# Kernel tuning notes

Hardware: AMD Instinct MI355X
Metric: run time of the kernel (lower is better)

Reference implementation:

```python
import math
import jax, jax.numpy as jnp
import numpy as np

B, N_IN, C_IN = 32, 16384, 64
IMG = 128            # sqrt(N_IN)
E_BR = 64            # embed_dim per PRM branch
DILATIONS = (1, 2, 3)
DIM = E_BR * len(DILATIONS)   # 192, attn input dim
EMB = 64             # token_dims * head_cnt
M_FEAT = int(EMB * 0.5)       # 32 performer random features
EPS = 1e-8


def setup_inputs() -> dict:
    key = jax.random.key(0)
    ks = jax.random.split(key, 12)
    x = jax.random.normal(ks[0], (B, N_IN, C_IN), jnp.float32)
    # PRM: one conv per dilation, weights stacked [nb, O, I, kh, kw] (OIHW)
    conv_w = jax.random.normal(ks[1], (len(DILATIONS), E_BR, C_IN, 3, 3), jnp.float32) * 0.05
    conv_b = jax.random.normal(ks[2], (len(DILATIONS), E_BR), jnp.float32) * 0.01
    ln1_g = jnp.ones((DIM,), jnp.float32)
    ln1_b = jnp.zeros((DIM,), jnp.float32)
    kqv_w = jax.random.normal(ks[3], (DIM, 3 * EMB), jnp.float32) * 0.02
    kqv_b = jnp.zeros((3 * EMB,), jnp.float32)
    proj_w = jax.random.normal(ks[4], (EMB, EMB), jnp.float32) * 0.02
    proj_b = jnp.zeros((EMB,), jnp.float32)
    # performer random-feature matrix: orthogonal rows, scaled by sqrt(m) (non-trainable)
    rng = np.random.default_rng(0)
    q, _ = np.linalg.qr(rng.standard_normal((EMB, M_FEAT)))
    w_perf = jnp.asarray(q.T * math.sqrt(M_FEAT), jnp.float32)  # [m, emb]
    ln2_g = jnp.ones((EMB,), jnp.float32)
    ln2_b = jnp.zeros((EMB,), jnp.float32)
    mlp_w1 = jax.random.normal(ks[5], (EMB, EMB), jnp.float32) * 0.02
    mlp_b1 = jnp.zeros((EMB,), jnp.float32)
    mlp_w2 = jax.random.normal(ks[6], (EMB, EMB), jnp.float32) * 0.02
    mlp_b2 = jnp.zeros((EMB,), jnp.float32)
    return dict(x=x, conv_w=conv_w, conv_b=conv_b, ln1_g=ln1_g, ln1_b=ln1_b,
                kqv_w=kqv_w, kqv_b=kqv_b, proj_w=proj_w, proj_b=proj_b,
                w_perf=w_perf, ln2_g=ln2_g, ln2_b=ln2_b,
                mlp_w1=mlp_w1, mlp_b1=mlp_b1, mlp_w2=mlp_w2, mlp_b2=mlp_b2)


def _layernorm(x, g, b):
    mu = jnp.mean(x, axis=-1, keepdims=True)
    var = jnp.var(x, axis=-1, keepdims=True)
    return (x - mu) * jax.lax.rsqrt(var + 1e-5) * g + b


def _prm_exp(t, w):
    # t: [B, T, emb], w: [m, emb] -> exp(w.t - |t|^2/2) / sqrt(m)
    xd = 0.5 * jnp.sum(t * t, axis=-1, keepdims=True)       # [B, T, 1]
    wtx = jnp.einsum('btd,md->btm', t, w)                    # [B, T, m]
    return jnp.exp(wtx - xd) / math.sqrt(w.shape[0])


def reference(x, conv_w, conv_b, ln1_g, ln1_b, kqv_w, kqv_b, proj_w, proj_b,
              w_perf, ln2_g, ln2_b, mlp_w1, mlp_b1, mlp_w2, mlp_b2):
    Bx, N, C = x.shape
    # x.permute(0,2,1) then reshape to image NCHW
    img = jnp.transpose(x, (0, 2, 1)).reshape(Bx, C, IMG, IMG)
    # PRM: multi-dilation strided convs + GELU, channel-concat (branch-major)
    ys = []
    for i, d in enumerate(DILATIONS):
        pad = d  # ceil(((k-1)*d + 1 - stride)/2) for k=3, stride=2
        y = jax.lax.conv_general_dilated(
            img, conv_w[i], window_strides=(2, 2),
            padding=[(pad, pad), (pad, pad)], rhs_dilation=(d, d),
            dimension_numbers=('NCHW', 'OIHW', 'NCHW'))
        y = y + conv_b[i][None, :, None, None]
        ys.append(jax.nn.gelu(y, approximate=False))
    y = jnp.concatenate(ys, axis=1)                          # [B, 3*E, H', W']
    tokens = jnp.transpose(y.reshape(Bx, DIM, -1), (0, 2, 1))  # [B, T, 192]

    # Token_performer.attn on norm1(tokens)
    h = _layernorm(tokens, ln1_g, ln1_b)
    kqv = h @ kqv_w + kqv_b                                  # [B, T, 3*emb]
    k, q, v = jnp.split(kqv, 3, axis=-1)                     # split order: k, q, v
    kp = _prm_exp(k, w_perf)                                 # [B, T, m]
    qp = _prm_exp(q, w_perf)                                 # [B, T, m]
    D = jnp.einsum('btm,bm->bt', qp, jnp.sum(kp, axis=1))[..., None]   # [B, T, 1]
    kptv = jnp.einsum('btd,btm->bdm', v, kp)                 # [B, emb, m]
    yatt = jnp.einsum('btm,bdm->btd', qp, kptv) / (D + EPS)  # [B, T, emb]
    yatt = v + (yatt @ proj_w + proj_b)                      # skip inside single_attn (dropout=id at eval)

    # x = x + drop_path(mlp(norm2(x))) ; drop_path/dropout = identity at eval
    h2 = _layernorm(yatt, ln2_g, ln2_b)
    h2 = jax.nn.gelu(h2 @ mlp_w1 + mlp_b1, approximate=False) @ mlp_w2 + mlp_b2
    return yatt + h2
```

## Files before the change

kernel.cpp:

```cpp
#include <hip/hip_runtime.h>
#include <hip/hip_bf16.h>


#define TOK 4096
#define NB  32

typedef __attribute__((ext_vector_type(8)))  short short8;
typedef __attribute__((ext_vector_type(4)))  short short4v;
typedef __attribute__((ext_vector_type(16))) float f32x16;

__device__ __forceinline__ float gelu_fast(float v) {
    float u = v * fmaf(0.0713548162f, v * v, 1.5957691216f);
    float e = __expf(-u);
    return v * __builtin_amdgcn_rcpf(1.f + e);
}

__device__ __forceinline__ short f2bf(float f) {
    __hip_bfloat16 h = __float2bfloat16(f);
    return *reinterpret_cast<short*>(&h);
}

__device__ __forceinline__ float bf2f(short s) {
    union { unsigned u; float f; } x;
    x.u = ((unsigned)(unsigned short)s) << 16;
    return x.f;
}

__global__ __launch_bounds__(256) void k_prep(
        const float* __restrict__ cw, const float* __restrict__ kw,
        const float* __restrict__ pw, const float* __restrict__ w1,
        const float* __restrict__ w2m, const float* __restrict__ wperf,
        short* __restrict__ w2c, short* __restrict__ kwbf,
        short* __restrict__ pTbf, short* __restrict__ w1bf,
        short* __restrict__ w2bf, short* __restrict__ wpbf) {
    int idx = blockIdx.x * 256 + threadIdx.x;
    if (idx < 110592) {
        int c = idx & 63;
        int t = idx >> 6;
        int e = t & 63;
        int tap = t >> 6;
        int kwi = tap % 3, t2 = tap / 3;
        int r = t2 % 3, brr = t2 / 3;
        float v = cw[(((brr * 64 + e) * 64 + c) * 3 + r) * 3 + kwi];
        int dst = ((((brr * 9 + r * 3 + kwi) * 4 + (c >> 4)) * 2 + ((c >> 3) & 1)) * 64 + e) * 8 + (c & 7);
        w2c[dst] = f2bf(v);
    } else if (idx < 147456) {
        int i2 = idx - 110592;
        int o = i2 / 192, i = i2 % 192;
        int dst = (((i >> 4) * 2 + ((i >> 3) & 1)) * 192 + o) * 8 + (i & 7);
        kwbf[dst] = f2bf(kw[i * 192 + o]);
    } else if (idx < 151552) {
        int i2 = idx - 147456;
        int o = i2 >> 6, d = i2 & 63;
        int dst = (((d >> 4) * 2 + ((d >> 3) & 1)) * 64 + o) * 8 + (d & 7);
        pTbf[dst] = f2bf(pw[d * 64 + o]);
    } else if (idx < 155648) {
        int i2 = idx - 151552;
        int i = i2 >> 6, jd = i2 & 63;
        int dst = (((jd >> 4) * 2 + ((jd >> 3) & 1)) * 64 + i) * 8 + (jd & 7);
        w1bf[dst] = f2bf(w1[jd * 64 + i]);
    } else if (idx < 159744) {
        int i2 = idx - 155648;
        int o = i2 >> 6, i = i2 & 63;
        int dst = (((i >> 4) * 2 + ((i >> 3) & 1)) * 64 + o) * 8 + (i & 7);
        w2bf[dst] = f2bf(w2m[i * 64 + o]);
    } else if (idx < 161792) {
        int i2 = idx - 159744;
        int m = i2 >> 6, d = i2 & 63;
        int dst = (((d >> 4) * 2 + ((d >> 3) & 1)) * 32 + m) * 8 + (d & 7);
        wpbf[dst] = f2bf(wperf[m * 64 + d]);
    }
}

__global__ __launch_bounds__(256) void k_conv6(
        const float* __restrict__ x, const short* __restrict__ w2c,
        const float* __restrict__ cb, short* __restrict__ tokens) {
    const int wg  = blockIdx.x;
    const int swz_id = (wg & 7) * 768 + (wg >> 3);
    const int b   = swz_id / 192;
    const int rem = swz_id - b * 192;
    const int oh  = rem / 3;
    const int br  = rem - oh * 3;
    const int d   = br + 1;
    const int tid = threadIdx.x;
    const int lane = tid & 63;
    const int wv = tid >> 6;
    const int cl = lane & 31;
    const int g  = lane >> 5;
    const int wm = wv & 1;
    const int wn = wv >> 1;

    __shared__ short sA[3 * 68 * 2 * 32];

    const int ow = wm * 32 + cl;
    const int ecol = wn * 32 + cl;
    const short* wbr = w2c + br * 9 * 4096;

    f32x16 acc = {0.f, 0.f, 0.f, 0.f, 0.f, 0.f, 0.f, 0.f,
                  0.f, 0.f, 0.f, 0.f, 0.f, 0.f, 0.f, 0.f};

    for (int h = 0; h < 2; ++h) {
        if (h == 0 && tid < 96) {
            int s16 = tid & 7;
            int ii  = (tid >> 3) & 3;
            int r   = tid >> 5;
            int i   = (ii < 2) ? ii : (64 + ii);
            short8 z = {0, 0, 0, 0, 0, 0, 0, 0};
            *(short8*)((char*)sA + (r * 68 + i) * 128 + s16 * 16) = z;
        }
        for (int it = 0; it < 6; ++it) {
            int flat = it * 256 + tid;
            int c8l = flat & 3;
            int iw  = (flat >> 2) & 127;
            int r   = flat >> 9;
            int ih  = 2 * oh + (r - 1) * d;
            int iw4 = iw + 4;
            int i   = iw4 >> 1;
            int p   = iw4 & 1;
            char* dst = (char*)sA + (r * 68 + i) * 128
                      + ((((p * 4 + c8l) * 16)) ^ ((i & 7) << 4));
            if ((unsigned)ih < 128u) {
                const float* src = x + ((size_t)(b * 16384 + ih * 128 + iw)) * 64
                                 + h * 32 + c8l * 8;
                float4 f0 = *(const float4*)(src);
                float4 f1 = *(const float4*)(src + 4);
                short8 v;
                v[0] = f2bf(f0.x); v[1] = f2bf(f0.y); v[2] = f2bf(f0.z); v[3] = f2bf(f0.w);
                v[4] = f2bf(f1.x); v[5] = f2bf(f1.y); v[6] = f2bf(f1.z); v[7] = f2bf(f1.w);
                *(short8*)dst = v;
            } else {
                short8 z = {0, 0, 0, 0, 0, 0, 0, 0};
                *(short8*)dst = z;
            }
        }
        __syncthreads();

#pragma unroll
        for (int r = 0; r < 3; ++r) {
#pragma unroll
            for (int kwi = 0; kwi < 3; ++kwi) {
                const int iw4 = 2 * ow + (kwi - 1) * d + 4;
                const int i   = iw4 >> 1;
                const int p   = iw4 & 1;
                const char* arow = (const char*)sA + (r * 68 + i) * 128;
                const int swzk = (i & 7) << 4;
                const short* wt = wbr + (r * 3 + kwi) * 4096;
#pragma unroll
                for (int kk = 0; kk < 2; ++kk) {
                    const int ks = h * 2 + kk;
                    short8 a = *(const short8*)(arow + ((((p * 4 + kk * 2 + g) * 16)) ^ swzk));
                    short8 bf = *(const short8*)(wt + ((ks * 2 + g) * 64 + ecol) * 8);
                    acc = __builtin_amdgcn_mfma_f32_32x32x16_bf16(a, bf, acc, 0, 0, 0);
                }
            }
        }
        __syncthreads();
    }

    const int eG = br * 64 + wn * 32 + cl;
    const float bias = cb[eG];
    short* outb = tokens + ((size_t)(b * TOK + oh * 64 + wm * 32)) * 192 + eG;
#pragma unroll
    for (int reg = 0; reg < 16; ++reg) {
        int owl = (reg & 3) + 8 * (reg >> 2) + 4 * g;
        outb[(size_t)owl * 192] = f2bf(gelu_fast(acc[reg] + bias));
    }
}

__global__ __launch_bounds__(256) void k_lnkqvp(
        const short* __restrict__ tokens, const float* __restrict__ g,
        const float* __restrict__ be, const short* __restrict__ wbf,
        const float* __restrict__ bias, const short* __restrict__ wpbf,
        short* __restrict__ vT, short* __restrict__ kpT,
        short* __restrict__ qpT) {
    const int b = blockIdx.y;
    const int t0 = blockIdx.x * 64;
    const int tid = threadIdx.x;

    __shared__ short sB[64 * 192];
    __shared__ float red[64 * 8];
    __shared__ float xdk[128];
    __shared__ float xdq[128];

    const int r = tid >> 2, q = tid & 3;
    const short* rowp = tokens + ((size_t)(b * TOK + t0 + r)) * 192 + q * 48;
    float v[48];
    float s1 = 0.f, s2 = 0.f;
#pragma unroll
    for (int i = 0; i < 6; ++i) {
        short8 x8 = *(const short8*)(rowp + i * 8);
#pragma unroll
        for (int j = 0; j < 8; ++j) {
            float f = bf2f(x8[j]);
            v[i * 8 + j] = f;
            s1 += f;
            s2 = fmaf(f, f, s2);
        }
    }
    red[r * 8 + q] = s1;
    red[r * 8 + 4 + q] = s2;
    __syncthreads();
    const float m1 = red[r * 8 + 0] + red[r * 8 + 1] + red[r * 8 + 2] + red[r * 8 + 3];
    const float m2 = red[r * 8 + 4] + red[r * 8 + 5] + red[r * 8 + 6] + red[r * 8 + 7];
    const float mu = m1 * (1.f / 192.f);
    const float var = m2 * (1.f / 192.f) - mu * mu;
    const float rs = rsqrtf(fmaxf(var, 0.f) + 1e-5f);
    const float4* g4 = (const float4*)(g + q * 48);
    const float4* b4 = (const float4*)(be + q * 48);
    char* rowB = (char*)sB + r * 384;
    const int swz = (r & 7) << 4;
#pragma unroll
    for (int i = 0; i < 12; ++i) {
        float4 gg = g4[i], bb = b4[i];
        short4v pk;
        pk.x = f2bf((v[4 * i + 0] - mu) * rs * gg.x + bb.x);
        pk.y = f2bf((v[4 * i + 1] - mu) * rs * gg.y + bb.y);
        pk.z = f2bf((v[4 * i + 2] - mu) * rs * gg.z + bb.z);
        pk.w = f2bf((v[4 * i + 3] - mu) * rs * gg.w + bb.w);
        *(short4v*)(rowB + (((q * 48 + i * 4) * 2) ^ swz)) = pk;
    }
    __syncthreads();

    const int lane = tid & 63;
    const int wv = tid >> 6;
    const int tt = wv & 1;
    const int wo = wv >> 1;
    const int colL = lane & 31;
    const int gq = lane >> 5;

    f32x16 acc0 = {0.f, 0.f, 0.f, 0.f, 0.f, 0.f, 0.f, 0.f,
                   0.f, 0.f, 0.f, 0.f, 0.f, 0.f, 0.f, 0.f};
    f32x16 acc1 = acc0, acc2 = acc0;
    const char* bbase = (const char*)sB + (tt * 32 + colL) * 384;
    const int bswz = ((tt * 32 + colL) & 7) << 4;
    const int ocol = wo * 32 + colL;

    for (int kk = 0; kk < 12; ++kk) {
        short8 bf = *(const short8*)(bbase + (((kk * 16 + gq * 8) * 2) ^ bswz));
        const short* ak = wbf + ((kk * 2 + gq) * 192 + ocol) * 8;
        short8 a0 = *(const short8*)(ak);
        short8 a1 = *(const short8*)(ak + 64 * 8);
        short8 a2 = *(const short8*)(ak + 128 * 8);
        acc0 = __builtin_amdgcn_mfma_f32_32x32x16_bf16(a0, bf, acc0, 0, 0, 0);
        acc1 = __builtin_amdgcn_mfma_f32_32x32x16_bf16(a1, bf, acc1, 0, 0, 0);
        acc2 = __builtin_amdgcn_mfma_f32_32x32x16_bf16(a2, bf, acc2, 0, 0, 0);
    }

    const int tl = tt * 32 + colL;
    const int tglob = t0 + tl;

    float kb[16], qb[16];
    float sk = 0.f, sq = 0.f;
    {
        short* vb = vT + (size_t)b * 64 * TOK + tglob;
#pragma unroll
        for (int reg = 0; reg < 16; ++reg) {
            int orow = (reg & 3) + 8 * (reg >> 2) + 4 * gq;
            int d = wo * 32 + orow;
            kb[reg] = acc0[reg] + bias[d];
            qb[reg] = acc1[reg] + bias[64 + d];
            float vv = acc2[reg] + bias[128 + d];
            vb[(size_t)d * TOK] = f2bf(vv);
            sk = fmaf(kb[reg], kb[reg], sk);
            sq = fmaf(qb[reg], qb[reg], sq);
        }
    }
    sk += __shfl_xor(sk, 32, 64);
    sq += __shfl_xor(sq, 32, 64);
    __syncthreads();

    if (gq == 0) {
        xdk[wo * 64 + tl] = 0.5f * sk;
        xdq[wo * 64 + tl] = 0.5f * sq;
    }
    {
        char* kS = (char*)sB;
        char* qS = (char*)sB + 8192;
        const int tswz = (tl & 7) << 4;
#pragma unroll
        for (int rq = 0; rq < 4; ++rq) {
            int d0 = wo * 32 + 8 * rq + 4 * gq;
            short4v pk, pq;
#pragma unroll
            for (int j = 0; j < 4; ++j) {
                ((short*)&pk)[j] = f2bf(kb[rq * 4 + j]);
                ((short*)&pq)[j] = f2bf(qb[rq * 4 + j]);
            }
            *(short4v*)(kS + tl * 128 + ((d0 * 2) ^ tswz)) = pk;
            *(short4v*)(qS + tl * 128 + ((d0 * 2) ^ tswz)) = pq;
        }
    }
    __syncthreads();

    {
        const int pass = wv >> 1;
        const int tt2 = wv & 1;
        const char* S = (char*)sB + pass * 8192;
        const int t2 = tt2 * 32 + colL;
        const int t2swz = (t2 & 7) << 4;
        f32x16 pacc = {0.f, 0.f, 0.f, 0.f, 0.f, 0.f, 0.f, 0.f,
                       0.f, 0.f, 0.f, 0.f, 0.f, 0.f, 0.f, 0.f};
#pragma unroll
        for (int ks = 0; ks < 4; ++ks) {
            short8 a = *(const short8*)(wpbf + ((ks * 2 + gq) * 32 + colL) * 8);
            short8 bb = *(const short8*)(S + t2 * 128 + (((ks * 16 + gq * 8) * 2) ^ t2swz));
            pacc = __builtin_amdgcn_mfma_f32_32x32x16_bf16(a, bb, pacc, 0, 0, 0);
        }
        const float* xda = pass ? xdq : xdk;
        const float xdv = xda[t2] + xda[64 + t2];
        short* dst = (pass ? qpT : kpT) + (size_t)b * 32 * TOK + t0 + t2;
#pragma unroll
        for (int reg = 0; reg < 16; ++reg) {
            int m = (reg & 3) + 8 * (reg >> 2) + 4 * gq;
            float kpv = __expf(pacc[reg] - xdv) * 0.17677669529663687f;
            dst[(size_t)m * TOK] = f2bf(kpv);
        }
    }
}

__global__ __launch_bounds__(256) void k_kptv(
        const short* __restrict__ vT, const short* __restrict__ kpT,
        float* __restrict__ kvp, float* __restrict__ skpp) {
    const int b = blockIdx.y, ch = blockIdx.x, tid = threadIdx.x;
    const int t = ch * 256 + tid;
    __shared__ float sv[256 * 65 + 256 * 36];
    float* skp = sv + 256 * 65;
    for (int dd = 0; dd < 64; ++dd)
        sv[tid * 65 + dd] = bf2f(vT[((size_t)(b * 64 + dd)) * TOK + t]);
    for (int m = 0; m < 32; ++m)
        skp[tid * 36 + m] = bf2f(kpT[((size_t)(b * 32 + m)) * TOK + t]);
    __syncthreads();

    const int dd = tid & 63;
    const int mg = __builtin_amdgcn_readfirstlane(tid >> 6);
    float acc[8];
#pragma unroll
    for (int j = 0; j < 8; ++j) acc[j] = 0.f;
    for (int tt = 0; tt < 256; ++tt) {
        float vv = sv[tt * 65 + dd];
        const float4* kq = (const float4*)(skp + tt * 36 + mg * 8);
        float4 a0 = kq[0], a1 = kq[1];
        acc[0] = fmaf(vv, a0.x, acc[0]);
        acc[1] = fmaf(vv, a0.y, acc[1]);
        acc[2] = fmaf(vv, a0.z, acc[2]);
        acc[3] = fmaf(vv, a0.w, acc[3]);
        acc[4] = fmaf(vv, a1.x, acc[4]);
        acc[5] = fmaf(vv, a1.y, acc[5]);
        acc[6] = fmaf(vv, a1.z, acc[6]);
        acc[7] = fmaf(vv, a1.w, acc[7]);
    }
    float* dst = kvp + (((size_t)(b * 16 + ch) * 64 + dd) * 32) + mg * 8;
#pragma unroll
    for (int j = 0; j < 8; ++j) dst[j] = acc[j];

    if (tid < 32) {
        float s = 0.f;
        for (int tt = 0; tt < 256; ++tt) s += skp[tt * 36 + tid];
        skpp[(b * 16 + ch) * 32 + tid] = s;
    }
}

__global__ __launch_bounds__(256) void k_reduce2(
        const float* __restrict__ kvp, const float* __restrict__ skpp,
        short* __restrict__ kvbf, float* __restrict__ sum_kp) {
    int idx = blockIdx.x * 256 + threadIdx.x;
    if (idx < 65536) {
        int b = idx >> 11, rem = idx & 2047, dd = rem >> 5, m = rem & 31;
        float s = 0.f;
        for (int ch = 0; ch < 16; ++ch) s += kvp[((b * 16 + ch) * 64 + dd) * 32 + m];
        int dst = (((b * 2 + (m >> 4)) * 2 + ((m >> 3) & 1)) * 64 + dd) * 8 + (m & 7);
        kvbf[dst] = f2bf(s);
    } else if (idx < 65536 + 1024) {
        int i = idx - 65536;
        int b = i >> 5, m = i & 31;
        float s = 0.f;
        for (int ch = 0; ch < 16; ++ch) s += skpp[(b * 16 + ch) * 32 + m];
        sum_kp[i] = s;
    }
}

__global__ __launch_bounds__(256) void k_fuse(
        const short* __restrict__ vT, const short* __restrict__ qpT,
        const short* __restrict__ kvbf, const float* __restrict__ sum_kp,
        const short* __restrict__ pTbf, const float* __restrict__ proj_b,
        const float* __restrict__ g2, const float* __restrict__ b2ln,
        const short* __restrict__ w1bf, const float* __restrict__ b1,
        const short* __restrict__ w2bf, const float* __restrict__ b2,
        float* __restrict__ out) {
    const int b = blockIdx.y;
    const int t0 = blockIdx.x * 64;
    const int tid = threadIdx.x;
    const int lane = tid & 63;
    const int cl = lane & 31;
    const int g  = lane >> 5;
    const int wv = tid >> 6;
    const int wr = wv & 1;
    const int wc = wv >> 1;

    __shared__ __align__(16) char pool[29952];
    short* qpS  = (short*)(pool + 0);
    short* ytS  = (short*)(pool + 5120);
    short* xnS  = (short*)(pool + 14336);
    short* hgS  = (short*)(pool + 0);
    float* outS = (float*)(pool + 9216);
    float* red  = (float*)(pool + 26624);
    float* stat = (float*)(pool + 27648);
    float* coefS= (float*)(pool + 28672);

    if (tid < 64) {
        coefS[tid]       = proj_b[tid];
        coefS[64 + tid]  = g2[tid];
        coefS[128 + tid] = b2ln[tid];
        coefS[192 + tid] = b1[tid];
        coefS[256 + tid] = b2[tid];
    }
    {
        const int t = tid & 63, q = tid >> 6;
        const float* sk = sum_kp + b * 32;
        float dsum = 0.f;
        short8 pk;
#pragma unroll
        for (int i = 0; i < 8; ++i) {
            int m = q * 8 + i;
            short s = qpT[((size_t)(b * 32 + m)) * TOK + t0 + t];
            dsum = fmaf(bf2f(s), sk[m], dsum);
            pk[i] = s;
        }
        *(short8*)(qpS + t * 40 + q * 8) = pk;
        red[t * 4 + q] = dsum;
    }
    __syncthreads();

    const int tl = wc * 32 + cl;
    const int tg = t0 + tl;
    const int rcol = wr * 32 + cl;

    f32x16 acc = {0.f, 0.f, 0.f, 0.f, 0.f, 0.f, 0.f, 0.f,
                  0.f, 0.f, 0.f, 0.f, 0.f, 0.f, 0.f, 0.f};
    {
        const short* Ab = kvbf + (size_t)b * 2048;
        short8 a0 = *(const short8*)(Ab + (g * 64 + rcol) * 8);
        short8 a1 = *(const short8*)(Ab + ((2 + g) * 64 + rcol) * 8);
        short8 b0 = *(const short8*)(qpS + tl * 40 + g * 8);
        short8 b1v = *(const short8*)(qpS + tl * 40 + 16 + g * 8);
        acc = __builtin_amdgcn_mfma_f32_32x32x16_bf16(a0, b0, acc, 0, 0, 0);
        acc = __builtin_amdgcn_mfma_f32_32x32x16_bf16(a1, b1v, acc, 0, 0, 0);
    }
    {
        float Dv = red[tl * 4 + 0] + red[tl * 4 + 1] + red[tl * 4 + 2] + red[tl * 4 + 3];
        float rD = 1.f / (Dv + 1e-8f);
#pragma unroll
        for (int rq = 0; rq < 4; ++rq) {
            int d0 = wr * 32 + 8 * rq + 4 * g;
            short4v p;
            p.x = f2bf(acc[rq * 4 + 0] * rD);
            p.y = f2bf(acc[rq * 4 + 1] * rD);
            p.z = f2bf(acc[rq * 4 + 2] * rD);
            p.w = f2bf(acc[rq * 4 + 3] * rD);
            *(short4v*)(ytS + tl * 72 + d0) = p;
        }
    }
    __syncthreads();

    f32x16 acc2 = {0.f, 0.f, 0.f, 0.f, 0.f, 0.f, 0.f, 0.f,
                   0.f, 0.f, 0.f, 0.f, 0.f, 0.f, 0.f, 0.f};
    {
#pragma unroll
        for (int ks = 0; ks < 4; ++ks) {
            short8 a = *(const short8*)(pTbf + ((ks * 2 + g) * 64 + rcol) * 8);
            short8 bb = *(const short8*)(ytS + tl * 72 + ks * 16 + g * 8);
            acc2 = __builtin_amdgcn_mfma_f32_32x32x16_bf16(a, bb, acc2, 0, 0, 0);
        }
    }
    float skv[16];
    {
        const short* vb = vT + (size_t)b * 64 * TOK + tg;
#pragma unroll
        for (int reg = 0; reg < 16; ++reg) {
            int o = wr * 32 + (reg & 3) + 8 * (reg >> 2) + 4 * g;
            skv[reg] = acc2[reg] + bf2f(vb[(size_t)o * TOK]) + coefS[o];
        }
    }

    {
        float s1 = 0.f, s2 = 0.f;
#pragma unroll
        for (int reg = 0; reg < 16; ++reg) {
            s1 += skv[reg];
            s2 = fmaf(skv[reg], skv[reg], s2);
        }
        s1 += __shfl_xor(s1, 32, 64);
        s2 += __shfl_xor(s2, 32, 64);
        if (g == 0) {
            stat[(wr * 64 + tl) * 2 + 0] = s1;
            stat[(wr * 64 + tl) * 2 + 1] = s2;
        }
        __syncthreads();
        float S1 = s1 + stat[((wr ^ 1) * 64 + tl) * 2 + 0];
        float S2 = s2 + stat[((wr ^ 1) * 64 + tl) * 2 + 1];
        float mu = S1 * (1.f / 64.f);
        float var = S2 * (1.f / 64.f) - mu * mu;
        float rs = rsqrtf(fmaxf(var, 0.f) + 1e-5f);
#pragma unroll
        for (int rq = 0; rq < 4; ++rq) {
            int o0 = wr * 32 + 8 * rq + 4 * g;
            short4v p;
#pragma unroll
            for (int j = 0; j < 4; ++j) {
                int o = o0 + j;
                float xn = (skv[rq * 4 + j] - mu) * rs * coefS[64 + o] + coefS[128 + o];
                ((short*)&p)[j] = f2bf(xn);
            }
            *(short4v*)(xnS + tl * 72 + o0) = p;
        }
    }
    __syncthreads();

    f32x16 acc3 = {0.f, 0.f, 0.f, 0.f, 0.f, 0.f, 0.f, 0.f,
                   0.f, 0.f, 0.f, 0.f, 0.f, 0.f, 0.f, 0.f};
    {
#pragma unroll
        for (int ks = 0; ks < 4; ++ks) {
            short8 a = *(const short8*)(w1bf + ((ks * 2 + g) * 64 + rcol) * 8);
            short8 bb = *(const short8*)(xnS + tl * 72 + ks * 16 + g * 8);
            acc3 = __builtin_amdgcn_mfma_f32_32x32x16_bf16(a, bb, acc3, 0, 0, 0);
        }
    }
    __syncthreads();
    {
#pragma unroll
        for (int rq = 0; rq < 4; ++rq) {
            int i0 = wr * 32 + 8 * rq + 4 * g;
            short4v p;
#pragma unroll
            for (int j = 0; j < 4; ++j) {
                int i = i0 + j;
                float hgv = gelu_fast(acc3[rq * 4 + j] + coefS[192 + i]);
                ((short*)&p)[j] = f2bf(hgv);
            }
            *(short4v*)(hgS + tl * 72 + i0) = p;
        }
    }
    __syncthreads();

    f32x16 acc4 = {0.f, 0.f, 0.f, 0.f, 0.f, 0.f, 0.f, 0.f,
                   0.f, 0.f, 0.f, 0.f, 0.f, 0.f, 0.f, 0.f};
    {
#pragma unroll
        for (int ks = 0; ks < 4; ++ks) {
            short8 a = *(const short8*)(w2bf + ((ks * 2 + g) * 64 + rcol) * 8);
            short8 bb = *(const short8*)(hgS + tl * 72 + ks * 16 + g * 8);
            acc4 = __builtin_amdgcn_mfma_f32_32x32x16_bf16(a, bb, acc4, 0, 0, 0);
        }
    }
    {
#pragma unroll
        for (int rq = 0; rq < 4; ++rq) {
            int o0 = wr * 32 + 8 * rq + 4 * g;
            float4 f;
#pragma unroll
            for (int j = 0; j < 4; ++j) {
                int o = o0 + j;
                ((float*)&f)[j] = skv[rq * 4 + j] + acc4[rq * 4 + j] + coefS[256 + o];
            }
            *(float4*)(outS + tl * 68 + o0) = f;
        }
    }
    __syncthreads();

    {
        const int tt = tid >> 2, qq = tid & 3;
        float* ob = out + ((size_t)(b * TOK) + t0 + tt) * 64;
#pragma unroll
        for (int it = 0; it < 4; ++it) {
            *(float4*)(ob + it * 16 + qq * 4) =
                *(float4*)(outS + tt * 68 + it * 16 + qq * 4);
        }
    }
}

extern "C" void kernel_launch(void* const* d_in, const int* in_sizes, int n_in,
                              void* d_out, int out_size, void* d_ws, size_t ws_size,
                              hipStream_t stream) {
    const float* x      = (const float*)d_in[0];
    const float* conv_w = (const float*)d_in[1];
    const float* conv_b = (const float*)d_in[2];
    const float* ln1_g  = (const float*)d_in[3];
    const float* ln1_b  = (const float*)d_in[4];
    const float* kqv_w  = (const float*)d_in[5];
    const float* kqv_b  = (const float*)d_in[6];
    const float* proj_w = (const float*)d_in[7];
    const float* proj_b = (const float*)d_in[8];
    const float* w_perf = (const float*)d_in[9];
    const float* ln2_g  = (const float*)d_in[10];
    const float* ln2_b  = (const float*)d_in[11];
    const float* mlp_w1 = (const float*)d_in[12];
    const float* mlp_b1 = (const float*)d_in[13];
    const float* mlp_w2 = (const float*)d_in[14];
    const float* mlp_b2 = (const float*)d_in[15];

    float* ws = (float*)d_ws;
    short* w2c    = (short*)ws;
    short* kwbf   = (short*)(ws + 55296);
    short* pTbf   = (short*)(ws + 73728);
    short* w1bf   = (short*)(ws + 75776);
    short* w2bf   = (short*)(ws + 77824);
    short* wpbf   = (short*)(ws + 79872);
    float* sum_kp = ws + 80896;
    short* kvbf   = (short*)(ws + 81920);
    short* tokens = (short*)(ws + 114688);
    float* wsB    = ws + 114688 + 12582912;
    short* vT     = (short*)wsB;
    short* qpT    = (short*)(wsB + 4194304);
    short* kpT    = (short*)(wsB + 6291456);
    float* skpp   = wsB + 8388608;
    float* kvp    = wsB + 8404992;
    float* outp   = (float*)d_out;

    k_prep   <<<632, 256, 0, stream>>>(conv_w, kqv_w, proj_w, mlp_w1, mlp_w2,
                                       w_perf, w2c, kwbf, pTbf, w1bf, w2bf, wpbf);
    k_conv6  <<<6144, 256, 0, stream>>>(x, w2c, conv_b, tokens);
    k_lnkqvp <<<dim3(64, 32), 256, 0, stream>>>(tokens, ln1_g, ln1_b, kwbf,
                                                kqv_b, wpbf, vT, kpT, qpT);
    k_kptv   <<<dim3(16, 32), 256, 0, stream>>>(vT, kpT, kvp, skpp);
    k_reduce2<<<260, 256, 0, stream>>>(kvp, skpp, kvbf, sum_kp);
    k_fuse   <<<dim3(64, 32), 256, 0, stream>>>(vT, qpT, kvbf, sum_kp,
                                                pTbf, proj_b, ln2_g, ln2_b,
                                                w1bf, mlp_b1, w2bf, mlp_b2, outp);
}
```

Before: 154.6 us.

## Compute two output rows per conv workgroup to reuse weight fragments

The dilated-conv kernel now has each workgroup produce two adjacent output rows with two accumulators, halving the grid. Each weight fragment loaded from global memory is reused for two MFMAs, and the channel loop is split into four phases of 16 channels with a new LDS layout and swizzle. This cuts redundant weight loads and per-workgroup overhead. In exchange there are more barriers per workgroup, more registers, and fewer workgroups to hide latency.

```diff
diff --git a/kernel.cpp b/kernel.cpp
--- a/kernel.cpp
+++ b/kernel.cpp
@@ -72,15 +72,16 @@
     }
 }
 
-__global__ __launch_bounds__(256) void k_conv6(
+__global__ __launch_bounds__(256) void k_conv7(
         const float* __restrict__ x, const short* __restrict__ w2c,
         const float* __restrict__ cb, short* __restrict__ tokens) {
     const int wg  = blockIdx.x;
-    const int swz_id = (wg & 7) * 768 + (wg >> 3);
-    const int b   = swz_id / 192;
-    const int rem = swz_id - b * 192;
-    const int oh  = rem / 3;
-    const int br  = rem - oh * 3;
+    const int swz_id = (wg & 7) * 384 + (wg >> 3);
+    const int b   = swz_id / 96;
+    const int rem = swz_id - b * 96;
+    const int ohp = rem / 3;
+    const int br  = rem - ohp * 3;
+    const int oh0 = ohp * 2;
     const int d   = br + 1;
     const int tid = threadIdx.x;
     const int lane = tid & 63;
@@ -90,38 +91,41 @@
     const int wm = wv & 1;
     const int wn = wv >> 1;
 
-    __shared__ short sA[3 * 68 * 2 * 32];
+    __shared__ short sA[6 * 34 * 64];
 
     const int ow = wm * 32 + cl;
     const int ecol = wn * 32 + cl;
     const short* wbr = w2c + br * 9 * 4096;
 
-    f32x16 acc = {0.f, 0.f, 0.f, 0.f, 0.f, 0.f, 0.f, 0.f,
-                  0.f, 0.f, 0.f, 0.f, 0.f, 0.f, 0.f, 0.f};
-
-    for (int h = 0; h < 2; ++h) {
-        if (h == 0 && tid < 96) {
-            int s16 = tid & 7;
-            int ii  = (tid >> 3) & 3;
-            int r   = tid >> 5;
-            int i   = (ii < 2) ? ii : (64 + ii);
-            short8 z = {0, 0, 0, 0, 0, 0, 0, 0};
-            *(short8*)((char*)sA + (r * 68 + i) * 128 + s16 * 16) = z;
-        }
+    f32x16 acc0 = {0.f, 0.f, 0.f, 0.f, 0.f, 0.f, 0.f, 0.f,
+                   0.f, 0.f, 0.f, 0.f, 0.f, 0.f, 0.f, 0.f};
+    f32x16 acc1 = acc0;
+
+    if (tid < 96) {
+        int slot = tid & 7;
+        int lsel = (tid >> 3) & 1;
+        int s    = tid >> 4;
+        int l    = lsel ? 33 : 0;
+        short8 z = {0, 0, 0, 0, 0, 0, 0, 0};
+        *(short8*)((char*)sA + (s * 34 + l) * 128 + slot * 16) = z;
+    }
+
+    for (int ph = 0; ph < 4; ++ph) {
         for (int it = 0; it < 6; ++it) {
             int flat = it * 256 + tid;
-            int c8l = flat & 3;
-            int iw  = (flat >> 2) & 127;
-            int r   = flat >> 9;
-            int ih  = 2 * oh + (r - 1) * d;
+            int c8 = flat & 1;
+            int iw = (flat >> 1) & 127;
+            int s  = flat >> 8;
+            int ohl = (s >= 3) ? 1 : 0;
+            int r   = s - ohl * 3;
+            int ih  = 2 * (oh0 + ohl) + (r - 1) * d;
             int iw4 = iw + 4;
-            int i   = iw4 >> 1;
-            int p   = iw4 & 1;
-            char* dst = (char*)sA + (r * 68 + i) * 128
-                      + ((((p * 4 + c8l) * 16)) ^ ((i & 7) << 4));
+            int l   = iw4 >> 2;
+            int slot = ((iw4 & 3) * 2 + c8) ^ (l & 7);
+            char* dst = (char*)sA + (s * 34 + l) * 128 + slot * 16;
             if ((unsigned)ih < 128u) {
                 const float* src = x + ((size_t)(b * 16384 + ih * 128 + iw)) * 64
-                                 + h * 32 + c8l * 8;
+                                 + ph * 16 + c8 * 8;
                 float4 f0 = *(const float4*)(src);
                 float4 f1 = *(const float4*)(src + 4);
                 short8 v;
@@ -139,18 +143,19 @@
         for (int r = 0; r < 3; ++r) {
 #pragma unroll
             for (int kwi = 0; kwi < 3; ++kwi) {
+                const short* wt = wbr + (r * 3 + kwi) * 4096;
+                short8 bfr = *(const short8*)(wt + ((ph * 2 + g) * 64 + ecol) * 8);
                 const int iw4 = 2 * ow + (kwi - 1) * d + 4;
-                const int i   = iw4 >> 1;
-                const int p   = iw4 & 1;
-                const char* arow = (const char*)sA + (r * 68 + i) * 128;
-                const int swzk = (i & 7) << 4;
-                const short* wt = wbr + (r * 3 + kwi) * 4096;
-#pragma unroll
-                for (int kk = 0; kk < 2; ++kk) {
-                    const int ks = h * 2 + kk;
-                    short8 a = *(const short8*)(arow + ((((p * 4 + kk * 2 + g) * 16)) ^ swzk));
-                    short8 bf = *(const short8*)(wt + ((ks * 2 + g) * 64 + ecol) * 8);
-                    acc = __builtin_amdgcn_mfma_f32_32x32x16_bf16(a, bf, acc, 0, 0, 0);
+                const int l   = iw4 >> 2;
+                const int slot = ((iw4 & 3) * 2 + g) ^ (l & 7);
+#pragma unroll
+                for (int ohl = 0; ohl < 2; ++ohl) {
+                    const int s = ohl * 3 + r;
+                    short8 a = *(const short8*)((char*)sA + (s * 34 + l) * 128 + slot * 16);
+                    if (ohl == 0)
+                        acc0 = __builtin_amdgcn_mfma_f32_32x32x16_bf16(a, bfr, acc0, 0, 0, 0);
+                    else
+                        acc1 = __builtin_amdgcn_mfma_f32_32x32x16_bf16(a, bfr, acc1, 0, 0, 0);
                 }
             }
         }
@@ -159,11 +164,21 @@
 
     const int eG = br * 64 + wn * 32 + cl;
     const float bias = cb[eG];
-    short* outb = tokens + ((size_t)(b * TOK + oh * 64 + wm * 32)) * 192 + eG;
-#pragma unroll
-    for (int reg = 0; reg < 16; ++reg) {
-        int owl = (reg & 3) + 8 * (reg >> 2) + 4 * g;
-        outb[(size_t)owl * 192] = f2bf(gelu_fast(acc[reg] + bias));
+    {
+        short* outb = tokens + ((size_t)(b * TOK + oh0 * 64 + wm * 32)) * 192 + eG;
+#pragma unroll
+        for (int reg = 0; reg < 16; ++reg) {
+            int owl = (reg & 3) + 8 * (reg >> 2) + 4 * g;
+            outb[(size_t)owl * 192] = f2bf(gelu_fast(acc0[reg] + bias));
+        }
+    }
+    {
+        short* outb = tokens + ((size_t)(b * TOK + (oh0 + 1) * 64 + wm * 32)) * 192 + eG;
+#pragma unroll
+        for (int reg = 0; reg < 16; ++reg) {
+            int owl = (reg & 3) + 8 * (reg >> 2) + 4 * g;
+            outb[(size_t)owl * 192] = f2bf(gelu_fast(acc1[reg] + bias));
+        }
     }
 }
 
@@ -619,7 +634,7 @@
 
     k_prep   <<<632, 256, 0, stream>>>(conv_w, kqv_w, proj_w, mlp_w1, mlp_w2,
                                        w_perf, w2c, kwbf, pTbf, w1bf, w2bf, wpbf);
-    k_conv6  <<<6144, 256, 0, stream>>>(x, w2c, conv_b, tokens);
+    k_conv7  <<<3072, 256, 0, stream>>>(x, w2c, conv_b, tokens);
     k_lnkqvp <<<dim3(64, 32), 256, 0, stream>>>(tokens, ln1_g, ln1_b, kwbf,
                                                 kqv_b, wpbf, vT, kpT, qpT);
     k_kptv   <<<dim3(16, 32), 256, 0, stream>>>(vT, kpT, kvp, skpp);
```

New measurement: 170.4 us. 10.2% more time.

## Pre-convert input to bf16 parity-split layout and drop LDS staging in conv

Applied to the files above, without the earlier changes.

Adds a pass that converts the fp32 input once into a bf16 layout split by column parity and channel slab. The conv kernel then loads MFMA A fragments directly from global memory, with no shared-memory staging or barriers, and zeros out-of-range taps with predication. This targets repeated fp32 reads and conversions across workgroups that share input rows. In exchange it adds a full extra write/read of the bf16 copy and uses strided global loads that depend on cache hits.

```diff
diff --git a/kernel.cpp b/kernel.cpp
--- a/kernel.cpp
+++ b/kernel.cpp
@@ -72,8 +72,34 @@
     }
 }
 
-__global__ __launch_bounds__(256) void k_conv6(
-        const float* __restrict__ x, const short* __restrict__ w2c,
+__global__ __launch_bounds__(256) void k_cvt2(
+        const float* __restrict__ x, short* __restrict__ xT) {
+    const int ih = blockIdx.x;
+    const int b  = blockIdx.y;
+    const float* rb = x + ((size_t)(b * 16384 + ih * 128)) * 64;
+    short* ob = xT + (size_t)(b * 128 + ih) * 8192;
+    const int tid = threadIdx.x;
+#pragma unroll
+    for (int it = 0; it < 4; ++it) {
+        int f = it * 256 + tid;
+        int j   = f & 7;
+        int s   = (f >> 3) & 7;
+        int whi = (f >> 6) & 7;
+        int par = f >> 9;
+        int iw2 = whi * 8 + j;
+        int iw  = 2 * iw2 + par;
+        const float* src = rb + iw * 64 + s * 8;
+        float4 f0 = *(const float4*)(src);
+        float4 f1 = *(const float4*)(src + 4);
+        short8 v;
+        v[0] = f2bf(f0.x); v[1] = f2bf(f0.y); v[2] = f2bf(f0.z); v[3] = f2bf(f0.w);
+        v[4] = f2bf(f1.x); v[5] = f2bf(f1.y); v[6] = f2bf(f1.z); v[7] = f2bf(f1.w);
+        *(short8*)(ob + ((par * 8 + s) * 64 + iw2) * 8) = v;
+    }
+}
+
+__global__ __launch_bounds__(256) void k_conv8(
+        const short* __restrict__ xT, const short* __restrict__ w2c,
         const float* __restrict__ cb, short* __restrict__ tokens) {
     const int wg  = blockIdx.x;
     const int swz_id = (wg & 7) * 768 + (wg >> 3);
@@ -89,72 +115,37 @@
     const int g  = lane >> 5;
     const int wm = wv & 1;
     const int wn = wv >> 1;
-
-    __shared__ short sA[3 * 68 * 2 * 32];
-
     const int ow = wm * 32 + cl;
     const int ecol = wn * 32 + cl;
     const short* wbr = w2c + br * 9 * 4096;
+    const short8 z8 = {0, 0, 0, 0, 0, 0, 0, 0};
 
     f32x16 acc = {0.f, 0.f, 0.f, 0.f, 0.f, 0.f, 0.f, 0.f,
                   0.f, 0.f, 0.f, 0.f, 0.f, 0.f, 0.f, 0.f};
 
-    for (int h = 0; h < 2; ++h) {
-        if (h == 0 && tid < 96) {
-            int s16 = tid & 7;
-            int ii  = (tid >> 3) & 3;
-            int r   = tid >> 5;
-            int i   = (ii < 2) ? ii : (64 + ii);
-            short8 z = {0, 0, 0, 0, 0, 0, 0, 0};
-            *(short8*)((char*)sA + (r * 68 + i) * 128 + s16 * 16) = z;
-        }
-        for (int it = 0; it < 6; ++it) {
-            int flat = it * 256 + tid;
-            int c8l = flat & 3;
-            int iw  = (flat >> 2) & 127;
-            int r   = flat >> 9;
-            int ih  = 2 * oh + (r - 1) * d;
-            int iw4 = iw + 4;
-            int i   = iw4 >> 1;
-            int p   = iw4 & 1;
-            char* dst = (char*)sA + (r * 68 + i) * 128
-                      + ((((p * 4 + c8l) * 16)) ^ ((i & 7) << 4));
-            if ((unsigned)ih < 128u) {
-                const float* src = x + ((size_t)(b * 16384 + ih * 128 + iw)) * 64
-                                 + h * 32 + c8l * 8;
-                float4 f0 = *(const float4*)(src);
-                float4 f1 = *(const float4*)(src + 4);
-                short8 v;
-                v[0] = f2bf(f0.x); v[1] = f2bf(f0.y); v[2] = f2bf(f0.z); v[3] = f2bf(f0.w);
-                v[4] = f2bf(f1.x); v[5] = f2bf(f1.y); v[6] = f2bf(f1.z); v[7] = f2bf(f1.w);
-                *(short8*)dst = v;
-            } else {
-                short8 z = {0, 0, 0, 0, 0, 0, 0, 0};
-                *(short8*)dst = z;
+#pragma unroll
+    for (int r = 0; r < 3; ++r) {
+        const int ih = 2 * oh + (r - 1) * d;
+        const bool rv = (unsigned)ih < 128u;
+        const int ihc = ih & 127;
+        const short* rowb = xT + (size_t)(b * 128 + ihc) * 8192;
+#pragma unroll
+        for (int kwi = 0; kwi < 3; ++kwi) {
+            const int o = (kwi - 1) * d;
+            const int par = o & 1;
+            const int iw2 = ow + ((o - par) >> 1);
+            const bool va = rv && ((unsigned)iw2 < 64u);
+            const int iw2c = iw2 & 63;
+            const short* abase = rowb + par * 4096 + iw2c * 8;
+            const short* wt = wbr + (r * 3 + kwi) * 4096;
+#pragma unroll
+            for (int ks = 0; ks < 4; ++ks) {
+                short8 a = *(const short8*)(abase + (ks * 2 + g) * 512);
+                if (!va) a = z8;
+                short8 bf = *(const short8*)(wt + ((ks * 2 + g) * 64 + ecol) * 8);
+                acc = __builtin_amdgcn_mfma_f32_32x32x16_bf16(a, bf, acc, 0, 0, 0);
             }
         }
-        __syncthreads();
-
-#pragma unroll
-        for (int r = 0; r < 3; ++r) {
-#pragma unroll
-            for (int kwi = 0; kwi < 3; ++kwi) {
-                const int iw4 = 2 * ow + (kwi - 1) * d + 4;
-                const int i   = iw4 >> 1;
-                const int p   = iw4 & 1;
-                const char* arow = (const char*)sA + (r * 68 + i) * 128;
-                const int swzk = (i & 7) << 4;
-                const short* wt = wbr + (r * 3 + kwi) * 4096;
-#pragma unroll
-                for (int kk = 0; kk < 2; ++kk) {
-                    const int ks = h * 2 + kk;
-                    short8 a = *(const short8*)(arow + ((((p * 4 + kk * 2 + g) * 16)) ^ swzk));
-                    short8 bf = *(const short8*)(wt + ((ks * 2 + g) * 64 + ecol) * 8);
-                    acc = __builtin_amdgcn_mfma_f32_32x32x16_bf16(a, bf, acc, 0, 0, 0);
-                }
-            }
-        }
-        __syncthreads();
     }
 
     const int eG = br * 64 + wn * 32 + cl;
@@ -615,11 +606,13 @@
     short* kpT    = (short*)(wsB + 6291456);
     float* skpp   = wsB + 8388608;
     float* kvp    = wsB + 8404992;
+    short* xT     = (short*)(ws + 114688 + 12582912 + 9453568);
     float* outp   = (float*)d_out;
 
     k_prep   <<<632, 256, 0, stream>>>(conv_w, kqv_w, proj_w, mlp_w1, mlp_w2,
                                        w_perf, w2c, kwbf, pTbf, w1bf, w2bf, wpbf);
-    k_conv6  <<<6144, 256, 0, stream>>>(x, w2c, conv_b, tokens);
+    k_cvt2   <<<dim3(128, 32), 256, 0, stream>>>(x, xT);
+    k_conv8  <<<6144, 256, 0, stream>>>(xT, w2c, conv_b, tokens);
     k_lnkqvp <<<dim3(64, 32), 256, 0, stream>>>(tokens, ln1_g, ln1_b, kwbf,
                                                 kqv_b, wpbf, vT, kpT, qpT);
     k_kptv   <<<dim3(16, 32), 256, 0, stream>>>(vT, kpT, kvp, skpp);
```

Measured after the change: 184.8 us. 1.19x slower.
